# Kernel optimization log

Measured on AMD Instinct MI355X. Metric: run time of the kernel, lower is better.

Reference implementation:

```python
import jax, jax.numpy as jnp
import numpy as np

B, S, V, H = 16, 256, 32, 256
LN_EPS = 1e-5


def setup_inputs() -> dict:
    key = jax.random.key(0)
    ks = jax.random.split(key, 8)
    sW = 1.0 / np.sqrt(H)
    return {
        "x": jax.random.normal(ks[0], (B, S, V, 1), jnp.float32),
        "W1": jax.random.normal(ks[1], (V, H), jnp.float32),          # linear1: input_size=1
        "b1": jax.random.normal(ks[2], (V, H), jnp.float32) * 0.1,
        "W2": jax.random.normal(ks[3], (V, H, H), jnp.float32) * sW,
        "b2": jax.random.normal(ks[4], (V, H), jnp.float32) * 0.1,
        "Wg": jax.random.normal(ks[5], (V, H, H), jnp.float32) * sW,
        "bg": jax.random.normal(ks[6], (V, H), jnp.float32) * 0.1,
        "gamma": jnp.ones((V, H), jnp.float32),
        "beta": jnp.zeros((V, H), jnp.float32),
        "Wa": jax.random.normal(ks[7], (H,), jnp.float32) * sW,
        "ba": jnp.zeros((1,), jnp.float32),
    }


def reference(x, W1, b1, W2, b2, Wg, bg, gamma, beta, Wa, ba):
    # Batched GRN over all variables at once (replaces the per-var Python loop).
    # x: [B,S,V,1]; linear1 with input_size=1 is a scalar-vector outer product.
    h = jax.nn.relu(x * W1 + b1)                                  # [B,S,V,H]
    h = jnp.einsum('bsvh,vhk->bsvk', h, W2) + b2                  # linear2
    gated = jax.nn.sigmoid(jnp.einsum('bsvh,vhk->bsvk', h, Wg) + bg) * h
    # residual is the raw scalar input (last dim 1), broadcast over H as in torch
    pre = x + gated                                               # [B,S,V,H]
    mu = jnp.mean(pre, axis=-1, keepdims=True)
    var = jnp.mean(jnp.square(pre - mu), axis=-1, keepdims=True)
    var_outputs = (pre - mu) * jax.lax.rsqrt(var + LN_EPS) * gamma + beta
    # softmax attention pooling over variables
    scores = jnp.einsum('bsvh,h->bsv', var_outputs, Wa) + ba[0]   # [B,S,V]
    attn = jax.nn.softmax(scores, axis=-1)[..., None]             # [B,S,V,1]
    vsn_out = jnp.sum(var_outputs * attn, axis=2)                 # [B,S,H]
    return vsn_out, attn
```

## Files before the change

### kernel.cpp

```cpp
#include <hip/hip_runtime.h>
#include <hip/hip_bf16.h>

typedef _Float16 f16;
typedef _Float16 f16x2 __attribute__((ext_vector_type(2)));
typedef _Float16 f16x4 __attribute__((ext_vector_type(4)));
typedef _Float16 f16x8 __attribute__((ext_vector_type(8)));
typedef float f32x4 __attribute__((ext_vector_type(4)));

#define T_TOK 4096
#define V_N 32
#define H_N 256
#define LN_EPS_F 1e-5f

__device__ __forceinline__ void gload16(const f16* g, f16* l) {
    __builtin_amdgcn_global_load_lds(
        (const __attribute__((address_space(1))) void*)g,
        (__attribute__((address_space(3))) void*)l, 16, 0, 0);
}
__device__ __forceinline__ void gload16f(const float* g, float* l) {
    __builtin_amdgcn_global_load_lds(
        (const __attribute__((address_space(1))) void*)g,
        (__attribute__((address_space(3))) void*)l, 16, 0, 0);
}

__global__ __launch_bounds__(256) void prep_transpose(
    const float* __restrict__ W2, const float* __restrict__ Wg,
    f16* __restrict__ W2t, f16* __restrict__ Wgt)
{
    __shared__ float tile[64][65];
    int bid = blockIdx.x;
    int w = bid >> 9;
    int rem = bid & 511;
    int v = rem >> 4;
    int kt = (rem >> 2) & 3;
    int nt = rem & 3;
    const float* src = w ? Wg : W2;
    f16* dst = w ? Wgt : W2t;
    const float* base = src + ((size_t)v * H_N + (size_t)kt * 64) * H_N + nt * 64;
    int tid = threadIdx.x;
    #pragma unroll
    for (int p = 0; p < 16; ++p) {
        int idx = p * 256 + tid;
        int r = idx >> 6, c = idx & 63;
        tile[r][c] = base[(size_t)r * H_N + c];
    }
    __syncthreads();
    f16* obase = dst + ((size_t)v * H_N + (size_t)nt * 64) * H_N + kt * 64;
    #pragma unroll
    for (int p = 0; p < 16; ++p) {
        int idx = p * 256 + tid;
        int r = idx >> 6, c = idx & 63;
        obase[(size_t)r * H_N + c] = (f16)tile[c][r];
    }
}

__global__ __launch_bounds__(256) void prep_w1(
    const float* __restrict__ W1, const float* __restrict__ b1,
    f16* __restrict__ W1h, f16* __restrict__ b1h)
{
    int i = blockIdx.x * 256 + threadIdx.x;
    W1h[i] = (f16)W1[i];
    b1h[i] = (f16)b1[i];
}

__global__ __launch_bounds__(512) void grn_h2(
    const float* __restrict__ x,
    const f16* __restrict__ W1h, const f16* __restrict__ b1h,
    const f16* __restrict__ W2t, const float* __restrict__ b2,
    f16* __restrict__ H2g)
{
    __shared__ f16 W2L[65536];
    __shared__ f16 W1L[256], b1L[256];
    __shared__ float b2L[256];

    int bid = blockIdx.x;
    int xcd = bid & 7, idx = bid >> 3;
    int v  = (xcd << 2) + (idx & 3);
    int t0 = (idx >> 2) * 512;
    int tid = threadIdx.x;
    int w = tid >> 6, lane = tid & 63;
    int lo = lane & 15, hi = lane >> 4;
    int q = w & 3, th = w >> 2;

    const f16* W2v = W2t + ((size_t)v << 16);

    int cs = (lane & 31) ^ ((w * 2 + (lane >> 5)) & 7);
    #pragma unroll
    for (int r = 0; r < 16; ++r)
        gload16(W2v + ((size_t)(r * 16 + w * 2 + (lane >> 5)) << 8) + (cs << 3),
                &W2L[(r * 16 + w * 2) << 8]);
    if (w == 0 && lane < 32) gload16(W1h + (v << 8) + (lane << 3), W1L);
    if (w == 1 && lane < 32) gload16(b1h + (v << 8) + (lane << 3), b1L);
    if (w == 2) gload16f(b2 + (v << 8) + (lane << 2), b2L);

    float xs[4][4];
    #pragma unroll
    for (int st = 0; st < 4; ++st)
        #pragma unroll
        for (int g = 0; g < 4; ++g)
            xs[st][g] = x[(size_t)(t0 + st * 128 + th * 64 + g * 16 + lo) * V_N + v];

    __syncthreads();

    #pragma unroll
    for (int st = 0; st < 4; ++st) {
        int m0 = t0 + st * 128 + th * 64;
        f16x8 x8[4];
        #pragma unroll
        for (int g = 0; g < 4; ++g) {
            f16 xh = (f16)xs[st][g];
            x8[g] = f16x8{ xh, xh, xh, xh, xh, xh, xh, xh };
        }
        f32x4 acc[4][4] = {};
        #pragma unroll
        for (int s = 0; s < 8; ++s) {
            f16x8 w8 = *(const f16x8*)&W1L[(s << 5) + (hi << 3)];
            f16x8 c8 = *(const f16x8*)&b1L[(s << 5) + (hi << 3)];
            f16x8 hv[4];
            #pragma unroll
            for (int g = 0; g < 4; ++g) {
                f16x8 t = x8[g] * w8 + c8;
                #pragma unroll
                for (int j = 0; j < 8; ++j) t[j] = t[j] > (f16)0 ? t[j] : (f16)0;
                hv[g] = t;
            }
            #pragma unroll
            for (int nf = 0; nf < 4; ++nf) {
                f16x8 af = *(const f16x8*)&W2L[((q * 64 + nf * 16 + lo) << 8)
                                               + ((((s << 2) + hi) ^ (lo & 7)) << 3)];
                #pragma unroll
                for (int g = 0; g < 4; ++g)
                    acc[g][nf] = __builtin_amdgcn_mfma_f32_16x16x32_f16(
                        af, hv[g], acc[g][nf], 0, 0, 0);
            }
        }
        #pragma unroll
        for (int nf = 0; nf < 4; ++nf) {
            int n0 = q * 64 + nf * 16 + (hi << 2);
            f32x4 b4 = *(const f32x4*)&b2L[n0];
            #pragma unroll
            for (int g = 0; g < 4; ++g) {
                f32x4 h = acc[g][nf] + b4;
                f16x4 hh = { (f16)h[0], (f16)h[1], (f16)h[2], (f16)h[3] };
                *(f16x4*)&H2g[((size_t)v * T_TOK + m0 + g * 16 + lo) * H_N + n0] = hh;
            }
        }
    }
}

__global__ __launch_bounds__(512) void grn_out(
    const f16* __restrict__ Wgt, const float* __restrict__ bg,
    const float* __restrict__ gamma, const float* __restrict__ beta,
    const float* __restrict__ Wa, const float* __restrict__ ba,
    const f16* H2g,
    f16* VOg,
    float* __restrict__ scores)
{
    __shared__ f16 WgL[65536];
    __shared__ float bgL[256], gmL[256], btL[256], waL[256];
    __shared__ float sqx[4][128][2];
    __shared__ float spxL[4][128];

    int bid = blockIdx.x;
    int xcd = bid & 7, idx = bid >> 3;
    int v  = (xcd << 2) + (idx & 3);
    int t0 = (idx >> 2) * 512;
    int tid = threadIdx.x;
    int w = tid >> 6, lane = tid & 63;
    int lo = lane & 15, hi = lane >> 4;
    int q = w & 3, th = w >> 2;

    const f16* Wgv = Wgt + ((size_t)v << 16);

    int cs = (lane & 31) ^ ((w * 2 + (lane >> 5)) & 7);
    #pragma unroll
    for (int r = 0; r < 16; ++r)
        gload16(Wgv + ((size_t)(r * 16 + w * 2 + (lane >> 5)) << 8) + (cs << 3),
                &WgL[(r * 16 + w * 2) << 8]);
    if (w == 0) gload16f(bg    + (v << 8) + (lane << 2), bgL);
    if (w == 1) gload16f(gamma + (v << 8) + (lane << 2), gmL);
    if (w == 2) gload16f(beta  + (v << 8) + (lane << 2), btL);
    if (w == 3) gload16f(Wa + (lane << 2), waL);
    float bav = ba[0];

    __syncthreads();

    #pragma unroll
    for (int st = 0; st < 4; ++st) {
        int m0 = t0 + st * 128 + th * 64;
        const f16* rp0 = H2g + ((size_t)v * T_TOK + m0 + 0 * 16 + lo) * H_N;
        const f16* rp1 = H2g + ((size_t)v * T_TOK + m0 + 1 * 16 + lo) * H_N;
        const f16* rp2 = H2g + ((size_t)v * T_TOK + m0 + 2 * 16 + lo) * H_N;
        const f16* rp3 = H2g + ((size_t)v * T_TOK + m0 + 3 * 16 + lo) * H_N;
        const f16* rp[4] = { rp0, rp1, rp2, rp3 };
        f16* vr0 = VOg + ((size_t)v * T_TOK + m0 + 0 * 16 + lo) * H_N;
        f16* vr1 = VOg + ((size_t)v * T_TOK + m0 + 1 * 16 + lo) * H_N;
        f16* vr2 = VOg + ((size_t)v * T_TOK + m0 + 2 * 16 + lo) * H_N;
        f16* vr3 = VOg + ((size_t)v * T_TOK + m0 + 3 * 16 + lo) * H_N;
        f16* vr[4] = { vr0, vr1, vr2, vr3 };

        f16x8 bf0[4], bf1[4], bf2[4];
        #pragma unroll
        for (int g = 0; g < 4; ++g) {
            bf0[g] = *(const f16x8*)&rp[g][0 * 32 + (hi << 3)];
            bf1[g] = *(const f16x8*)&rp[g][1 * 32 + (hi << 3)];
            bf2[g] = *(const f16x8*)&rp[g][2 * 32 + (hi << 3)];
        }
        f32x4 acc[4][4] = {};

#define BSTEP(BF, S)                                                             \
        {                                                                        \
            _Pragma("unroll")                                                    \
            for (int nf = 0; nf < 4; ++nf) {                                     \
                f16x8 af = *(const f16x8*)&WgL[((q * 64 + nf * 16 + lo) << 8)    \
                                     + (((((S) << 2) + hi) ^ (lo & 7)) << 3)];   \
                _Pragma("unroll")                                                \
                for (int g = 0; g < 4; ++g)                                      \
                    acc[g][nf] = __builtin_amdgcn_mfma_f32_16x16x32_f16(         \
                        af, BF[g], acc[g][nf], 0, 0, 0);                         \
            }                                                                    \
            if ((S) < 5) {                                                       \
                _Pragma("unroll")                                                \
                for (int g = 0; g < 4; ++g)                                      \
                    BF[g] = *(const f16x8*)&rp[g][((S) + 3) * 32 + (hi << 3)];   \
            }                                                                    \
        }

        BSTEP(bf0, 0) BSTEP(bf1, 1) BSTEP(bf2, 2)
        BSTEP(bf0, 3) BSTEP(bf1, 4) BSTEP(bf2, 5)
        BSTEP(bf0, 6) BSTEP(bf1, 7)
#undef BSTEP

        float sr[4] = {}, qr[4] = {};
        #pragma unroll
        for (int g = 0; g < 4; ++g) {
            #pragma unroll
            for (int nf = 0; nf < 4; ++nf) {
                int n0 = q * 64 + nf * 16 + (hi << 2);
                f32x4 bgv = *(const f32x4*)&bgL[n0];
                f16x4 h2v = *(const f16x4*)&rp[g][n0];
                #pragma unroll
                for (int r = 0; r < 4; ++r) {
                    float a = acc[g][nf][r] + bgv[r];
                    float sg = 1.f / (1.f + __expf(-a));
                    float val = sg * (float)h2v[r];
                    acc[g][nf][r] = val;
                    sr[g] += val; qr[g] += val * val;
                }
            }
            sr[g] += __shfl_xor(sr[g], 16); sr[g] += __shfl_xor(sr[g], 32);
            qr[g] += __shfl_xor(qr[g], 16); qr[g] += __shfl_xor(qr[g], 32);
        }
        if (hi == 0) {
            #pragma unroll
            for (int g = 0; g < 4; ++g) {
                sqx[q][th * 64 + g * 16 + lo][0] = sr[g];
                sqx[q][th * 64 + g * 16 + lo][1] = qr[g];
            }
        }
        __syncthreads();
        float mu[4], inv[4];
        #pragma unroll
        for (int g = 0; g < 4; ++g) {
            int tk = th * 64 + g * 16 + lo;
            float s_ = sqx[0][tk][0] + sqx[1][tk][0] + sqx[2][tk][0] + sqx[3][tk][0];
            float q_ = sqx[0][tk][1] + sqx[1][tk][1] + sqx[2][tk][1] + sqx[3][tk][1];
            mu[g] = s_ * (1.f / 256.f);
            float var = q_ * (1.f / 256.f) - mu[g] * mu[g];
            inv[g] = rsqrtf(var + LN_EPS_F);
        }
        float sp[4] = {};
        #pragma unroll
        for (int g = 0; g < 4; ++g) {
            #pragma unroll
            for (int nf = 0; nf < 4; ++nf) {
                int n0 = q * 64 + nf * 16 + (hi << 2);
                f32x4 gm = *(const f32x4*)&gmL[n0];
                f32x4 bt = *(const f32x4*)&btL[n0];
                f32x4 wa = *(const f32x4*)&waL[n0];
                f16x4 ov;
                #pragma unroll
                for (int r = 0; r < 4; ++r) {
                    float o = (acc[g][nf][r] - mu[g]) * inv[g] * gm[r] + bt[r];
                    sp[g] += o * wa[r];
                    ov[r] = (f16)o;
                }
                *(f16x4*)&vr[g][n0] = ov;
            }
            sp[g] += __shfl_xor(sp[g], 16); sp[g] += __shfl_xor(sp[g], 32);
        }
        if (hi == 0) {
            #pragma unroll
            for (int g = 0; g < 4; ++g) spxL[q][th * 64 + g * 16 + lo] = sp[g];
        }
        __syncthreads();
        if (q == 0 && hi == 0) {
            #pragma unroll
            for (int g = 0; g < 4; ++g) {
                int tk = th * 64 + g * 16 + lo;
                scores[(size_t)(t0 + st * 128 + tk) * V_N + v] =
                    spxL[0][tk] + spxL[1][tk] + spxL[2][tk] + spxL[3][tk] + bav;
            }
        }
    }
}

__global__ __launch_bounds__(128) void pool(
    const f16* __restrict__ VO,
    const float* __restrict__ scores,
    float* __restrict__ out)
{
    int t = blockIdx.x, tid = threadIdx.x;
    __shared__ float sc[V_N];
    if (tid < V_N) sc[tid] = scores[t * V_N + tid];
    __syncthreads();
    float mx = -1e30f;
    #pragma unroll
    for (int v = 0; v < V_N; ++v) mx = fmaxf(mx, sc[v]);
    float e[V_N];
    float sum = 0.f;
    #pragma unroll
    for (int v = 0; v < V_N; ++v) { e[v] = __expf(sc[v] - mx); sum += e[v]; }
    float isum = 1.f / sum;
    float a0 = 0.f, a1 = 0.f;
    #pragma unroll
    for (int v = 0; v < V_N; ++v) {
        f16x2 vv = *(const f16x2*)&VO[((size_t)v * T_TOK + t) * H_N + tid * 2];
        float ww = e[v] * isum;
        a0 = fmaf((float)vv[0], ww, a0);
        a1 = fmaf((float)vv[1], ww, a1);
    }
    *(float2*)&out[(size_t)t * H_N + tid * 2] = make_float2(a0, a1);
    if (tid < V_N)
        out[(size_t)T_TOK * H_N + (size_t)t * V_N + tid] = e[tid] * isum;
}

extern "C" void kernel_launch(void* const* d_in, const int* in_sizes, int n_in,
                              void* d_out, int out_size, void* d_ws, size_t ws_size,
                              hipStream_t stream)
{
    const float* x     = (const float*)d_in[0];
    const float* W1    = (const float*)d_in[1];
    const float* b1    = (const float*)d_in[2];
    const float* W2    = (const float*)d_in[3];
    const float* b2    = (const float*)d_in[4];
    const float* Wg    = (const float*)d_in[5];
    const float* bg    = (const float*)d_in[6];
    const float* gamma = (const float*)d_in[7];
    const float* beta  = (const float*)d_in[8];
    const float* Wa    = (const float*)d_in[9];
    const float* ba    = (const float*)d_in[10];
    float* out = (float*)d_out;

    char* ws = (char*)d_ws;
    f16* W2t = (f16*)ws;
    f16* Wgt = (f16*)(ws + ((size_t)4 << 20));
    f16* H2g = (f16*)(ws + ((size_t)8 << 20));
    float* scores = (float*)(ws + ((size_t)72 << 20));
    f16* W1h = (f16*)(ws + ((size_t)72 << 20) + (512 << 10));
    f16* b1h = (f16*)(ws + ((size_t)72 << 20) + (528 << 10));
    const size_t NEED = ((size_t)137 << 20);
    f16* VOg = (ws_size >= NEED) ? (f16*)(ws + ((size_t)73 << 20)) : H2g;

    prep_transpose<<<1024, 256, 0, stream>>>(W2, Wg, W2t, Wgt);
    prep_w1<<<32, 256, 0, stream>>>(W1, b1, W1h, b1h);
    grn_h2<<<256, 512, 0, stream>>>(x, W1h, b1h, W2t, b2, H2g);
    grn_out<<<256, 512, 0, stream>>>(Wgt, bg, gamma, beta, Wa, ba, H2g, VOg, scores);
    pool<<<4096, 128, 0, stream>>>(VOg, scores, out);
}
```

Measured before the change: 127.2 us.

## Hold Wg in registers and double-buffer H2 tiles through LDS in grn_out

```diff
diff --git a/kernel.cpp b/kernel.cpp
--- a/kernel.cpp
+++ b/kernel.cpp
@@ -148,7 +148,7 @@
     }
 }
 
-__global__ __launch_bounds__(512) void grn_out(
+__global__ __launch_bounds__(512, 2) void grn_out(
     const f16* __restrict__ Wgt, const float* __restrict__ bg,
     const float* __restrict__ gamma, const float* __restrict__ beta,
     const float* __restrict__ Wa, const float* __restrict__ ba,
@@ -156,89 +156,81 @@
     f16* VOg,
     float* __restrict__ scores)
 {
-    __shared__ f16 WgL[65536];
+    __shared__ __align__(16) f16 H2L[2][64 * 256];
     __shared__ float bgL[256], gmL[256], btL[256], waL[256];
-    __shared__ float sqx[4][128][2];
-    __shared__ float spxL[4][128];
+    __shared__ float sqx[8][4][16][2];
+    __shared__ float spxL[8][4][16];
 
     int bid = blockIdx.x;
     int xcd = bid & 7, idx = bid >> 3;
     int v  = (xcd << 2) + (idx & 3);
-    int t0 = (idx >> 2) * 512;
+    int t0 = (idx >> 2) * 256;
     int tid = threadIdx.x;
     int w = tid >> 6, lane = tid & 63;
     int lo = lane & 15, hi = lane >> 4;
-    int q = w & 3, th = w >> 2;
 
     const f16* Wgv = Wgt + ((size_t)v << 16);
 
-    int cs = (lane & 31) ^ ((w * 2 + (lane >> 5)) & 7);
-    #pragma unroll
-    for (int r = 0; r < 16; ++r)
-        gload16(Wgv + ((size_t)(r * 16 + w * 2 + (lane >> 5)) << 8) + (cs << 3),
-                &WgL[(r * 16 + w * 2) << 8]);
+    f16x8 afW[8][2];
+    #pragma unroll
+    for (int s = 0; s < 8; ++s)
+        #pragma unroll
+        for (int nf = 0; nf < 2; ++nf)
+            afW[s][nf] = *(const f16x8*)&Wgv[((w * 32 + nf * 16 + lo) << 8)
+                                             + (s << 5) + (hi << 3)];
+
     if (w == 0) gload16f(bg    + (v << 8) + (lane << 2), bgL);
     if (w == 1) gload16f(gamma + (v << 8) + (lane << 2), gmL);
     if (w == 2) gload16f(beta  + (v << 8) + (lane << 2), btL);
     if (w == 3) gload16f(Wa + (lane << 2), waL);
     float bav = ba[0];
 
-    __syncthreads();
-
-    #pragma unroll
-    for (int st = 0; st < 4; ++st) {
-        int m0 = t0 + st * 128 + th * 64;
-        const f16* rp0 = H2g + ((size_t)v * T_TOK + m0 + 0 * 16 + lo) * H_N;
-        const f16* rp1 = H2g + ((size_t)v * T_TOK + m0 + 1 * 16 + lo) * H_N;
-        const f16* rp2 = H2g + ((size_t)v * T_TOK + m0 + 2 * 16 + lo) * H_N;
-        const f16* rp3 = H2g + ((size_t)v * T_TOK + m0 + 3 * 16 + lo) * H_N;
-        const f16* rp[4] = { rp0, rp1, rp2, rp3 };
-        f16* vr0 = VOg + ((size_t)v * T_TOK + m0 + 0 * 16 + lo) * H_N;
-        f16* vr1 = VOg + ((size_t)v * T_TOK + m0 + 1 * 16 + lo) * H_N;
-        f16* vr2 = VOg + ((size_t)v * T_TOK + m0 + 2 * 16 + lo) * H_N;
-        f16* vr3 = VOg + ((size_t)v * T_TOK + m0 + 3 * 16 + lo) * H_N;
-        f16* vr[4] = { vr0, vr1, vr2, vr3 };
-
-        f16x8 bf0[4], bf1[4], bf2[4];
+    auto stage = [&](int tile, int buf) {
+        #pragma unroll
+        for (int i = 0; i < 4; ++i) {
+            int r = w * 8 + i * 2 + (lane >> 5);
+            int cg = (lane & 31) ^ (r & 31);
+            gload16(H2g + ((size_t)v * T_TOK + t0 + tile * 64 + r) * H_N + (cg << 3),
+                    &H2L[buf][(w * 8 + i * 2) << 8]);
+        }
+    };
+
+    stage(0, 0);
+    asm volatile("s_waitcnt vmcnt(0) lgkmcnt(0)" ::: "memory");
+    __builtin_amdgcn_s_barrier();
+
+    #pragma unroll
+    for (int t = 0; t < 4; ++t) {
+        const int buf = t & 1;
+        if (t < 3) stage(t + 1, buf ^ 1);
+        int m0 = t0 + t * 64;
+
+        f32x4 acc[4][2] = {};
+        #pragma unroll
+        for (int s = 0; s < 8; ++s) {
+            #pragma unroll
+            for (int g = 0; g < 4; ++g) {
+                int tok = g * 16 + lo;
+                int slot = ((s << 2) + hi) ^ (tok & 31);
+                f16x8 bf = *(const f16x8*)&H2L[buf][(tok << 8) + (slot << 3)];
+                acc[g][0] = __builtin_amdgcn_mfma_f32_16x16x32_f16(
+                    afW[s][0], bf, acc[g][0], 0, 0, 0);
+                acc[g][1] = __builtin_amdgcn_mfma_f32_16x16x32_f16(
+                    afW[s][1], bf, acc[g][1], 0, 0, 0);
+            }
+        }
+
+        float sr[4] = {}, qr[4] = {};
         #pragma unroll
         for (int g = 0; g < 4; ++g) {
-            bf0[g] = *(const f16x8*)&rp[g][0 * 32 + (hi << 3)];
-            bf1[g] = *(const f16x8*)&rp[g][1 * 32 + (hi << 3)];
-            bf2[g] = *(const f16x8*)&rp[g][2 * 32 + (hi << 3)];
-        }
-        f32x4 acc[4][4] = {};
-
-#define BSTEP(BF, S)                                                             \
-        {                                                                        \
-            _Pragma("unroll")                                                    \
-            for (int nf = 0; nf < 4; ++nf) {                                     \
-                f16x8 af = *(const f16x8*)&WgL[((q * 64 + nf * 16 + lo) << 8)    \
-                                     + (((((S) << 2) + hi) ^ (lo & 7)) << 3)];   \
-                _Pragma("unroll")                                                \
-                for (int g = 0; g < 4; ++g)                                      \
-                    acc[g][nf] = __builtin_amdgcn_mfma_f32_16x16x32_f16(         \
-                        af, BF[g], acc[g][nf], 0, 0, 0);                         \
-            }                                                                    \
-            if ((S) < 5) {                                                       \
-                _Pragma("unroll")                                                \
-                for (int g = 0; g < 4; ++g)                                      \
-                    BF[g] = *(const f16x8*)&rp[g][((S) + 3) * 32 + (hi << 3)];   \
-            }                                                                    \
-        }
-
-        BSTEP(bf0, 0) BSTEP(bf1, 1) BSTEP(bf2, 2)
-        BSTEP(bf0, 3) BSTEP(bf1, 4) BSTEP(bf2, 5)
-        BSTEP(bf0, 6) BSTEP(bf1, 7)
-#undef BSTEP
-
-        float sr[4] = {}, qr[4] = {};
-        #pragma unroll
-        for (int g = 0; g < 4; ++g) {
-            #pragma unroll
-            for (int nf = 0; nf < 4; ++nf) {
-                int n0 = q * 64 + nf * 16 + (hi << 2);
+            int tok = g * 16 + lo;
+            #pragma unroll
+            for (int nf = 0; nf < 2; ++nf) {
+                int n0 = w * 32 + nf * 16 + (hi << 2);
                 f32x4 bgv = *(const f32x4*)&bgL[n0];
-                f16x4 h2v = *(const f16x4*)&rp[g][n0];
+                int slot = ((w << 2) + (nf << 1) + (hi >> 1)) ^ (tok & 31);
+                f16x4 h2v = *(const f16x4*)&H2L[buf][(tok << 8) + (slot << 3)
+                                                     + ((hi & 1) << 2)];
                 #pragma unroll
                 for (int r = 0; r < 4; ++r) {
                     float a = acc[g][nf][r] + bgv[r];
@@ -254,27 +246,33 @@
         if (hi == 0) {
             #pragma unroll
             for (int g = 0; g < 4; ++g) {
-                sqx[q][th * 64 + g * 16 + lo][0] = sr[g];
-                sqx[q][th * 64 + g * 16 + lo][1] = qr[g];
+                sqx[w][g][lo][0] = sr[g];
+                sqx[w][g][lo][1] = qr[g];
             }
         }
         __syncthreads();
+
         float mu[4], inv[4];
         #pragma unroll
         for (int g = 0; g < 4; ++g) {
-            int tk = th * 64 + g * 16 + lo;
-            float s_ = sqx[0][tk][0] + sqx[1][tk][0] + sqx[2][tk][0] + sqx[3][tk][0];
-            float q_ = sqx[0][tk][1] + sqx[1][tk][1] + sqx[2][tk][1] + sqx[3][tk][1];
-            mu[g] = s_ * (1.f / 256.f);
-            float var = q_ * (1.f / 256.f) - mu[g] * mu[g];
+            float st = 0.f, qt = 0.f;
+            #pragma unroll
+            for (int ww = 0; ww < 8; ++ww) {
+                st += sqx[ww][g][lo][0];
+                qt += sqx[ww][g][lo][1];
+            }
+            mu[g] = st * (1.f / 256.f);
+            float var = qt * (1.f / 256.f) - mu[g] * mu[g];
             inv[g] = rsqrtf(var + LN_EPS_F);
         }
+
         float sp[4] = {};
         #pragma unroll
         for (int g = 0; g < 4; ++g) {
-            #pragma unroll
-            for (int nf = 0; nf < 4; ++nf) {
-                int n0 = q * 64 + nf * 16 + (hi << 2);
+            f16* VOr = VOg + ((size_t)v * T_TOK + m0 + g * 16 + lo) * H_N;
+            #pragma unroll
+            for (int nf = 0; nf < 2; ++nf) {
+                int n0 = w * 32 + nf * 16 + (hi << 2);
                 f32x4 gm = *(const f32x4*)&gmL[n0];
                 f32x4 bt = *(const f32x4*)&btL[n0];
                 f32x4 wa = *(const f32x4*)&waL[n0];
@@ -285,21 +283,24 @@
                     sp[g] += o * wa[r];
                     ov[r] = (f16)o;
                 }
-                *(f16x4*)&vr[g][n0] = ov;
+                *(f16x4*)&VOr[n0] = ov;
             }
             sp[g] += __shfl_xor(sp[g], 16); sp[g] += __shfl_xor(sp[g], 32);
         }
         if (hi == 0) {
             #pragma unroll
-            for (int g = 0; g < 4; ++g) spxL[q][th * 64 + g * 16 + lo] = sp[g];
-        }
-        __syncthreads();
-        if (q == 0 && hi == 0) {
-            #pragma unroll
-            for (int g = 0; g < 4; ++g) {
-                int tk = th * 64 + g * 16 + lo;
-                scores[(size_t)(t0 + st * 128 + tk) * V_N + v] =
-                    spxL[0][tk] + spxL[1][tk] + spxL[2][tk] + spxL[3][tk] + bav;
+            for (int g = 0; g < 4; ++g) spxL[w][g][lo] = sp[g];
+        }
+        asm volatile("s_waitcnt vmcnt(8) lgkmcnt(0)" ::: "memory");
+        __builtin_amdgcn_s_barrier();
+
+        if (w == 0 && hi == 0) {
+            #pragma unroll
+            for (int g = 0; g < 4; ++g) {
+                float tsum = bav;
+                #pragma unroll
+                for (int ww = 0; ww < 8; ++ww) tsum += spxL[ww][g][lo];
+                scores[(size_t)(m0 + g * 16 + lo) * V_N + v] = tsum;
             }
         }
     }
@@ -365,6 +366,6 @@
     prep_transpose<<<1024, 256, 0, stream>>>(W2, Wg, W2t, Wgt);
     prep_w1<<<32, 256, 0, stream>>>(W1, b1, W1h, b1h);
     grn_h2<<<256, 512, 0, stream>>>(x, W1h, b1h, W2t, b2, H2g);
-    grn_out<<<256, 512, 0, stream>>>(Wgt, bg, gamma, beta, Wa, ba, H2g, VOg, scores);
+    grn_out<<<512, 512, 0, stream>>>(Wgt, bg, gamma, beta, Wa, ba, H2g, VOg, scores);
     pool<<<4096, 128, 0, stream>>>(VOg, scores, out);
 }
```

Measured after the change: 119.7 us. 1.06x faster.
